# Optimization experiments

Measured on AMD Instinct MI355X. Metric: run time of the kernel, lower is better.

## Reference

```python
import jax, jax.numpy as jnp
import numpy as np

TEMP_UPDATE = 1e-05
EPS = 1e-12  # torch F.normalize eps


def _l2norm(x, axis):
    n = jnp.sqrt(jnp.sum(x * x, axis=axis, keepdims=True))
    return x / jnp.maximum(n, EPS)


def setup_inputs() -> dict:
    key = jax.random.key(0)
    k1, k2 = jax.random.split(key)
    query = jax.random.normal(k1, (64, 256, 512), dtype=jnp.float32)
    keys = jax.random.normal(k2, (2048, 512), dtype=jnp.float32)
    return {"query": query, "keys": keys}


def reference(query, keys):
    bs, t, d = query.shape
    m = keys.shape[0]
    # F.normalize(query, dim=2)
    q = _l2norm(query, axis=2)
    qr = q.reshape(bs * t, d)                      # [N, d]
    score = qr @ keys.T                            # [N, m]
    score_query = jax.nn.softmax(score, axis=0)    # softmax over queries per slot
    score_memory = jax.nn.softmax(score, axis=1)   # softmax over slots per query
    # topk(1) over memory dim -> argmax slot per query
    g = jnp.argmax(score_memory, axis=1)           # [N] int
    col_max = jnp.max(score_query, axis=0)         # [m]
    # weight per query: score_query[n, g_n] / max(score_query[:, g_n])
    w = jnp.take_along_axis(score_query, g[:, None], axis=1)[:, 0] / col_max[g]
    # fused scatter-add replacing the per-slot python loop
    query_update = jax.ops.segment_sum(w[:, None] * qr, g, num_segments=m)  # [m, d]
    updated = _l2norm(TEMP_UPDATE * query_update + keys, axis=1)
    return jax.lax.stop_gradient(updated)  # original returns .detach()
```

## Files before the change

kernel.cpp:

```cpp
#include <hip/hip_runtime.h>
#include <math.h>

#define N_Q     16384
#define DDIM    512
#define M_SLOTS 2048
#define EPSN    1e-12f
#define TEMPU   1e-5f
#define KSCALE  25.4f
#define QSCALE  127.0f
#define INV_S   (1.0f / (127.0f * 25.4f))

typedef unsigned int u32;
typedef unsigned long long u64;
typedef __attribute__((ext_vector_type(4))) int i32x4;

__device__ __forceinline__ void gld_lds16(const void* g, void* l) {
    __builtin_amdgcn_global_load_lds(
        (const __attribute__((address_space(1))) u32*)(g),
        (__attribute__((address_space(3))) u32*)(l), 16, 0, 0);
}
__device__ __forceinline__ float block_reduce_sum_128(float v, float* sred, int t) {
    #pragma unroll
    for (int o = 32; o > 0; o >>= 1) v += __shfl_down(v, o, 64);
    if ((t & 63) == 0) sred[t >> 6] = v;
    __syncthreads();
    return sred[0] + sred[1];
}
__device__ __forceinline__ char q8(float x, float s) {
    int v = __float2int_rn(x * s);
    v = v < -127 ? -127 : (v > 127 ? 127 : v);
    return (char)v;
}

__global__ __launch_bounds__(128) void k_prep(const float* __restrict__ q,
                                              const float* __restrict__ keys,
                                              char* __restrict__ qi8,
                                              char* __restrict__ ki8) {
    __shared__ float sred[2];
    int b = blockIdx.x;
    int t = threadIdx.x;
    if (b < N_Q) {
        float4 v = ((const float4*)(q + (size_t)b * DDIM))[t];
        float ss = v.x * v.x + v.y * v.y + v.z * v.z + v.w * v.w;
        ss = block_reduce_sum_128(ss, sred, t);
        float s = QSCALE / fmaxf(sqrtf(ss), EPSN);
        char4 o;
        o.x = q8(v.x, s);
        o.y = q8(v.y, s);
        o.z = q8(v.z, s);
        o.w = q8(v.w, s);
        ((char4*)(qi8 + (size_t)b * DDIM))[t] = o;
    } else {
        int r = b - N_Q;
        float4 v = ((const float4*)(keys + (size_t)r * DDIM))[t];
        char4 o;
        o.x = q8(v.x, KSCALE);
        o.y = q8(v.y, KSCALE);
        o.z = q8(v.z, KSCALE);
        o.w = q8(v.w, KSCALE);
        ((char4*)(ki8 + (size_t)r * DDIM))[t] = o;
    }
}

__global__ __launch_bounds__(256) void k_score(const char* __restrict__ qi8,
                                               const char* __restrict__ ki8,
                                               u64* __restrict__ rowpack,
                                               int* __restrict__ colmax) {
    __shared__ char sA[2][128 * 64];
    __shared__ char sB[2][128 * 64];

    int t = threadIdx.x;
    int lane = t & 63;
    int wid = t >> 6;
    int wrow = wid >> 1;
    int wcol = wid & 1;
    int lr = lane & 15;
    int kc = lane >> 4;

    int n0 = blockIdx.y * 128;
    int j0 = blockIdx.x * 128;

    int srow = t >> 2;
    int scolB = (t & 3) * 16;

    const char* gA0 = qi8 + (size_t)(n0 + srow) * DDIM + scolB;
    const char* gA1 = qi8 + (size_t)(n0 + 64 + srow) * DDIM + scolB;
    const char* gB0 = ki8 + (size_t)(j0 + srow) * DDIM + scolB;
    const char* gB1 = ki8 + (size_t)(j0 + 64 + srow) * DDIM + scolB;

    i32x4 acc[4][4] = {};

#define STAGE(buf, k0)  do {                                   \
        gld_lds16(gA0 + (k0), &sA[buf][t * 16]);               \
        gld_lds16(gA1 + (k0), &sA[buf][4096 + t * 16]);        \
        gld_lds16(gB0 + (k0), &sB[buf][t * 16]);               \
        gld_lds16(gB1 + (k0), &sB[buf][4096 + t * 16]);        \
    } while (0)

    STAGE(0, 0);
    __syncthreads();

    #pragma unroll
    for (int kt = 0; kt < 8; ++kt) {
        const int cur = kt & 1;
        if (kt < 7) STAGE(cur ^ 1, (kt + 1) * 64);

        i32x4 a[4], b[4];
        #pragma unroll
        for (int i = 0; i < 4; ++i)
            a[i] = *(const i32x4*)&sA[cur][(wrow * 64 + i * 16 + lr) * 64 + kc * 16];
        #pragma unroll
        for (int j = 0; j < 4; ++j)
            b[j] = *(const i32x4*)&sB[cur][(wcol * 64 + j * 16 + lr) * 64 + kc * 16];
        #pragma unroll
        for (int i = 0; i < 4; ++i)
            #pragma unroll
            for (int j = 0; j < 4; ++j)
                acc[i][j] = __builtin_amdgcn_mfma_i32_16x16x64_i8(a[i], b[j], acc[i][j], 0, 0, 0);

        if (kt < 7) __syncthreads();
    }
#undef STAGE

    #pragma unroll
    for (int i = 0; i < 4; ++i) {
        #pragma unroll
        for (int r = 0; r < 4; ++r) {
            int v = acc[i][0][r];
            int c = j0 + wcol * 64 + lr;
            #pragma unroll
            for (int j = 1; j < 4; ++j) {
                int vj = acc[i][j][r];
                int cj = j0 + wcol * 64 + j * 16 + lr;
                if (vj > v) { v = vj; c = cj; }
            }
            #pragma unroll
            for (int off = 1; off < 16; off <<= 1) {
                int ov = __shfl_xor(v, off, 64);
                int oc = __shfl_xor(c, off, 64);
                if (ov > v || (ov == v && oc < c)) { v = ov; c = oc; }
            }
            if (lr == 0) {
                int grow = n0 + wrow * 64 + i * 16 + kc * 4 + r;
                u64 pk = ((u64)(u32)(v ^ 0x80000000) << 32) | (u64)(~(u32)c);
                atomicMax(rowpack + grow, pk);
            }
        }
    }
    #pragma unroll
    for (int j = 0; j < 4; ++j) {
        int m = acc[0][j][0];
        #pragma unroll
        for (int i = 0; i < 4; ++i)
            #pragma unroll
            for (int r = 0; r < 4; ++r) m = max(m, acc[i][j][r]);
        m = max(m, __shfl_xor(m, 16, 64));
        m = max(m, __shfl_xor(m, 32, 64));
        if (kc == 0) atomicMax(colmax + j0 + wcol * 64 + j * 16 + lr, m);
    }
}

__global__ __launch_bounds__(256) void k_hist(const u64* __restrict__ rowpack,
                                              u32* __restrict__ cnt) {
    int n = blockIdx.x * 256 + threadIdx.x;
    u64 p = rowpack[n];
    int g = (int)(~(u32)(p & 0xFFFFFFFFull));
    atomicAdd(cnt + g, 1u);
}

__global__ __launch_bounds__(256) void k_scan(const u32* __restrict__ cnt,
                                              u32* __restrict__ start,
                                              u32* __restrict__ cursor) {
    __shared__ u32 wsum[4];
    int t = threadIdx.x;
    int lane = t & 63, w = t >> 6;
    u32 local[8], s = 0;
    #pragma unroll
    for (int i = 0; i < 8; ++i) { local[i] = cnt[t * 8 + i]; s += local[i]; }
    u32 x = s;
    #pragma unroll
    for (int off = 1; off < 64; off <<= 1) {
        u32 y = __shfl_up(x, off, 64);
        if (lane >= off) x += y;
    }
    if (lane == 63) wsum[w] = x;
    __syncthreads();
    u32 base = 0;
    #pragma unroll
    for (int i = 0; i < 4; ++i) if (i < w) base += wsum[i];
    u32 run = base + x - s;
    #pragma unroll
    for (int i = 0; i < 8; ++i) {
        start[t * 8 + i] = run;
        cursor[t * 8 + i] = run;
        run += local[i];
    }
}

__global__ __launch_bounds__(256) void k_fill(const u64* __restrict__ rowpack,
                                              const int* __restrict__ colmax,
                                              u32* __restrict__ cursor,
                                              u32* __restrict__ perm,
                                              float* __restrict__ wval) {
    int n = blockIdx.x * 256 + threadIdx.x;
    u64 p = rowpack[n];
    int vi = (int)(((u32)(p >> 32)) ^ 0x80000000u);
    int g = (int)(~(u32)(p & 0xFFFFFFFFull));
    int cm = colmax[g];
    float w = expf((float)(vi - cm) * INV_S);
    u32 pos = atomicAdd(cursor + g, 1u);
    perm[pos] = (u32)n;
    wval[pos] = w;
}

__global__ __launch_bounds__(128) void k_gather_final(const char* __restrict__ qi8,
                                                      const u32* __restrict__ start,
                                                      const u32* __restrict__ cnt,
                                                      const u32* __restrict__ perm,
                                                      const float* __restrict__ wval,
                                                      const float* __restrict__ keys,
                                                      float* __restrict__ out) {
    __shared__ float sred[2];
    int j = blockIdx.x;
    int t = threadIdx.x;
    u32 s = start[j];
    u32 e = s + cnt[j];
    float ax = 0.f, ay = 0.f, az = 0.f, aw = 0.f;
    for (u32 i = s; i < e; ++i) {
        u32 n = perm[i];
        float wq = wval[i] * (1.0f / 127.0f);
        char4 q4 = ((const char4*)(qi8 + (size_t)n * DDIM))[t];
        ax = fmaf(wq, (float)q4.x, ax);
        ay = fmaf(wq, (float)q4.y, ay);
        az = fmaf(wq, (float)q4.z, az);
        aw = fmaf(wq, (float)q4.w, aw);
    }
    float4 k4 = ((const float4*)(keys + (size_t)j * DDIM))[t];
    float4 v;
    v.x = fmaf(TEMPU, ax, k4.x);
    v.y = fmaf(TEMPU, ay, k4.y);
    v.z = fmaf(TEMPU, az, k4.z);
    v.w = fmaf(TEMPU, aw, k4.w);
    float ss = v.x * v.x + v.y * v.y + v.z * v.z + v.w * v.w;
    ss = block_reduce_sum_128(ss, sred, t);
    float inv = 1.0f / fmaxf(sqrtf(ss), EPSN);
    v.x *= inv; v.y *= inv; v.z *= inv; v.w *= inv;
    ((float4*)(out + (size_t)j * DDIM))[t] = v;
}

extern "C" void kernel_launch(void* const* d_in, const int* in_sizes, int n_in,
                              void* d_out, int out_size, void* d_ws, size_t ws_size,
                              hipStream_t stream) {
    const float* query = (const float*)d_in[0];
    const float* keys  = (const float*)d_in[1];
    float* out = (float*)d_out;

    char* ws = (char*)d_ws;
    const size_t OFF_QI8   = 0;
    const size_t OFF_ROW   = 8388608;
    const size_t OFF_CNT   = OFF_ROW + 131072;
    const size_t OFF_CMAX  = OFF_CNT + 8192;
    const size_t OFF_START = OFF_CMAX + 8192;
    const size_t OFF_CUR   = OFF_START + 8192;
    const size_t OFF_PERM  = OFF_CUR + 8192;
    const size_t OFF_W     = OFF_PERM + 65536;
    const size_t OFF_KI8   = OFF_W + 65536;

    char*   qi8    = ws + OFF_QI8;
    u64*    rowpack= (u64*)(ws + OFF_ROW);
    u32*    cnt    = (u32*)(ws + OFF_CNT);
    int*    cmax   = (int*)(ws + OFF_CMAX);
    u32*    start  = (u32*)(ws + OFF_START);
    u32*    cursor = (u32*)(ws + OFF_CUR);
    u32*    perm   = (u32*)(ws + OFF_PERM);
    float*  wval   = (float*)(ws + OFF_W);
    char*   ki8    = ws + OFF_KI8;

    hipMemsetAsync(ws + OFF_ROW, 0, 131072 + 8192, stream);
    hipMemsetAsync(ws + OFF_CMAX, 0x80, 8192, stream);

    k_prep<<<N_Q + M_SLOTS, 128, 0, stream>>>(query, keys, qi8, ki8);

    dim3 g2(M_SLOTS / 128, N_Q / 128);
    k_score<<<g2, 256, 0, stream>>>(qi8, ki8, rowpack, cmax);

    k_hist<<<N_Q / 256, 256, 0, stream>>>(rowpack, cnt);
    k_scan<<<1, 256, 0, stream>>>(cnt, start, cursor);
    k_fill<<<N_Q / 256, 256, 0, stream>>>(rowpack, cmax, cursor, perm, wval);
    k_gather_final<<<M_SLOTS, 128, 0, stream>>>(qi8, start, cnt, perm, wval, keys, out);
}
```

Before: 86.97 us.

## Triple-buffer score GEMM loads and fuse hist/scan/fill into one LDS sort kernel

```diff
diff --git a/kernel.cpp b/kernel.cpp
--- a/kernel.cpp
+++ b/kernel.cpp
@@ -65,9 +65,9 @@
 __global__ __launch_bounds__(256) void k_score(const char* __restrict__ qi8,
                                                const char* __restrict__ ki8,
                                                u64* __restrict__ rowpack,
-                                               int* __restrict__ colmax) {
-    __shared__ char sA[2][128 * 64];
-    __shared__ char sB[2][128 * 64];
+                                               u32* __restrict__ colmax) {
+    __shared__ char sA[3][128 * 64];
+    __shared__ char sB[3][128 * 64];
 
     int t = threadIdx.x;
     int lane = t & 63;
@@ -98,12 +98,15 @@
     } while (0)
 
     STAGE(0, 0);
-    __syncthreads();
+    STAGE(1, 64);
+    asm volatile("s_waitcnt vmcnt(4)" ::: "memory");
+    __builtin_amdgcn_s_barrier();
+    __builtin_amdgcn_sched_barrier(0);
 
     #pragma unroll
     for (int kt = 0; kt < 8; ++kt) {
-        const int cur = kt & 1;
-        if (kt < 7) STAGE(cur ^ 1, (kt + 1) * 64);
+        const int cur = kt % 3;
+        if (kt < 6) STAGE((kt + 2) % 3, (kt + 2) * 64);
 
         i32x4 a[4], b[4];
         #pragma unroll
@@ -118,7 +121,12 @@
             for (int j = 0; j < 4; ++j)
                 acc[i][j] = __builtin_amdgcn_mfma_i32_16x16x64_i8(a[i], b[j], acc[i][j], 0, 0, 0);
 
-        if (kt < 7) __syncthreads();
+        if (kt < 6)       asm volatile("s_waitcnt vmcnt(4)" ::: "memory");
+        else if (kt == 6) asm volatile("s_waitcnt vmcnt(0)" ::: "memory");
+        if (kt < 7) {
+            __builtin_amdgcn_s_barrier();
+            __builtin_amdgcn_sched_barrier(0);
+        }
     }
 #undef STAGE
 
@@ -156,27 +164,38 @@
             for (int r = 0; r < 4; ++r) m = max(m, acc[i][j][r]);
         m = max(m, __shfl_xor(m, 16, 64));
         m = max(m, __shfl_xor(m, 32, 64));
-        if (kc == 0) atomicMax(colmax + j0 + wcol * 64 + j * 16 + lr, m);
-    }
-}
-
-__global__ __launch_bounds__(256) void k_hist(const u64* __restrict__ rowpack,
-                                              u32* __restrict__ cnt) {
-    int n = blockIdx.x * 256 + threadIdx.x;
-    u64 p = rowpack[n];
-    int g = (int)(~(u32)(p & 0xFFFFFFFFull));
-    atomicAdd(cnt + g, 1u);
-}
-
-__global__ __launch_bounds__(256) void k_scan(const u32* __restrict__ cnt,
-                                              u32* __restrict__ start,
-                                              u32* __restrict__ cursor) {
-    __shared__ u32 wsum[4];
+        if (kc == 0) atomicMax(colmax + j0 + wcol * 64 + j * 16 + lr,
+                               (u32)m ^ 0x80000000u);
+    }
+}
+
+__global__ __launch_bounds__(1024) void k_sort(const u64* __restrict__ rowpack,
+                                               const u32* __restrict__ colmax,
+                                               u32* __restrict__ start_g,
+                                               u32* __restrict__ cnt_g,
+                                               u32* __restrict__ perm,
+                                               float* __restrict__ wval) {
+    __shared__ u32 scnt[M_SLOTS];
+    __shared__ u32 scur[M_SLOTS];
+    __shared__ u32 wsum[16];
     int t = threadIdx.x;
     int lane = t & 63, w = t >> 6;
-    u32 local[8], s = 0;
-    #pragma unroll
-    for (int i = 0; i < 8; ++i) { local[i] = cnt[t * 8 + i]; s += local[i]; }
+
+    scnt[t] = 0;
+    scnt[t + 1024] = 0;
+    __syncthreads();
+
+    #pragma unroll
+    for (int i = 0; i < 16; ++i) {
+        int n = i * 1024 + t;
+        u64 p = rowpack[n];
+        int g = (int)(~(u32)(p & 0xFFFFFFFFull));
+        atomicAdd(&scnt[g], 1u);
+    }
+    __syncthreads();
+
+    u32 c0 = scnt[2 * t], c1 = scnt[2 * t + 1];
+    u32 s = c0 + c1;
     u32 x = s;
     #pragma unroll
     for (int off = 1; off < 64; off <<= 1) {
@@ -185,32 +204,33 @@
     }
     if (lane == 63) wsum[w] = x;
     __syncthreads();
-    u32 base = 0;
-    #pragma unroll
-    for (int i = 0; i < 4; ++i) if (i < w) base += wsum[i];
-    u32 run = base + x - s;
-    #pragma unroll
-    for (int i = 0; i < 8; ++i) {
-        start[t * 8 + i] = run;
-        cursor[t * 8 + i] = run;
-        run += local[i];
-    }
-}
-
-__global__ __launch_bounds__(256) void k_fill(const u64* __restrict__ rowpack,
-                                              const int* __restrict__ colmax,
-                                              u32* __restrict__ cursor,
-                                              u32* __restrict__ perm,
-                                              float* __restrict__ wval) {
-    int n = blockIdx.x * 256 + threadIdx.x;
-    u64 p = rowpack[n];
-    int vi = (int)(((u32)(p >> 32)) ^ 0x80000000u);
-    int g = (int)(~(u32)(p & 0xFFFFFFFFull));
-    int cm = colmax[g];
-    float w = expf((float)(vi - cm) * INV_S);
-    u32 pos = atomicAdd(cursor + g, 1u);
-    perm[pos] = (u32)n;
-    wval[pos] = w;
+    if (t == 0) {
+        u32 a = 0;
+        #pragma unroll
+        for (int i = 0; i < 16; ++i) { u32 v = wsum[i]; wsum[i] = a; a += v; }
+    }
+    __syncthreads();
+    u32 ex = wsum[w] + x - s;
+    scur[2 * t]     = ex;
+    scur[2 * t + 1] = ex + c0;
+    start_g[2 * t]     = ex;
+    start_g[2 * t + 1] = ex + c0;
+    cnt_g[2 * t]     = c0;
+    cnt_g[2 * t + 1] = c1;
+    __syncthreads();
+
+    #pragma unroll
+    for (int i = 0; i < 16; ++i) {
+        int n = i * 1024 + t;
+        u64 p = rowpack[n];
+        int vi = (int)(((u32)(p >> 32)) ^ 0x80000000u);
+        int g = (int)(~(u32)(p & 0xFFFFFFFFull));
+        int cm = (int)(colmax[g] ^ 0x80000000u);
+        float wq = expf((float)(vi - cm) * INV_S);
+        u32 pos = atomicAdd(&scur[g], 1u);
+        perm[pos] = (u32)n;
+        wval[pos] = wq;
+    }
 }
 
 __global__ __launch_bounds__(128) void k_gather_final(const char* __restrict__ qi8,
@@ -258,34 +278,29 @@
     char* ws = (char*)d_ws;
     const size_t OFF_QI8   = 0;
     const size_t OFF_ROW   = 8388608;
-    const size_t OFF_CNT   = OFF_ROW + 131072;
-    const size_t OFF_CMAX  = OFF_CNT + 8192;
+    const size_t OFF_CMAX  = OFF_ROW + 131072;
     const size_t OFF_START = OFF_CMAX + 8192;
-    const size_t OFF_CUR   = OFF_START + 8192;
-    const size_t OFF_PERM  = OFF_CUR + 8192;
+    const size_t OFF_CNT   = OFF_START + 8192;
+    const size_t OFF_PERM  = OFF_CNT + 8192;
     const size_t OFF_W     = OFF_PERM + 65536;
     const size_t OFF_KI8   = OFF_W + 65536;
 
     char*   qi8    = ws + OFF_QI8;
     u64*    rowpack= (u64*)(ws + OFF_ROW);
+    u32*    cmax   = (u32*)(ws + OFF_CMAX);
+    u32*    start  = (u32*)(ws + OFF_START);
     u32*    cnt    = (u32*)(ws + OFF_CNT);
-    int*    cmax   = (int*)(ws + OFF_CMAX);
-    u32*    start  = (u32*)(ws + OFF_START);
-    u32*    cursor = (u32*)(ws + OFF_CUR);
     u32*    perm   = (u32*)(ws + OFF_PERM);
     float*  wval   = (float*)(ws + OFF_W);
     char*   ki8    = ws + OFF_KI8;
 
     hipMemsetAsync(ws + OFF_ROW, 0, 131072 + 8192, stream);
-    hipMemsetAsync(ws + OFF_CMAX, 0x80, 8192, stream);
 
     k_prep<<<N_Q + M_SLOTS, 128, 0, stream>>>(query, keys, qi8, ki8);
 
     dim3 g2(M_SLOTS / 128, N_Q / 128);
     k_score<<<g2, 256, 0, stream>>>(qi8, ki8, rowpack, cmax);
 
-    k_hist<<<N_Q / 256, 256, 0, stream>>>(rowpack, cnt);
-    k_scan<<<1, 256, 0, stream>>>(cnt, start, cursor);
-    k_fill<<<N_Q / 256, 256, 0, stream>>>(rowpack, cmax, cursor, perm, wval);
+    k_sort<<<1, 1024, 0, stream>>>(rowpack, cmax, start, cnt, perm, wval);
     k_gather_final<<<M_SLOTS, 128, 0, stream>>>(qi8, start, cnt, perm, wval, keys, out);
 }
```

Measured after the change: 103.0 us. 18.4% more time.

## Stage full key tile in LDS once and stream query fragments from registers

Applied to the files above, without the earlier changes.

```diff
diff --git a/kernel.cpp b/kernel.cpp
--- a/kernel.cpp
+++ b/kernel.cpp
@@ -65,9 +65,8 @@
 __global__ __launch_bounds__(256) void k_score(const char* __restrict__ qi8,
                                                const char* __restrict__ ki8,
                                                u64* __restrict__ rowpack,
-                                               int* __restrict__ colmax) {
-    __shared__ char sA[2][128 * 64];
-    __shared__ char sB[2][128 * 64];
+                                               u32* __restrict__ colmax) {
+    __shared__ char sB[128 * 512];
 
     int t = threadIdx.x;
     int lane = t & 63;
@@ -80,47 +79,46 @@
     int n0 = blockIdx.y * 128;
     int j0 = blockIdx.x * 128;
 
-    int srow = t >> 2;
-    int scolB = (t & 3) * 16;
-
-    const char* gA0 = qi8 + (size_t)(n0 + srow) * DDIM + scolB;
-    const char* gA1 = qi8 + (size_t)(n0 + 64 + srow) * DDIM + scolB;
-    const char* gB0 = ki8 + (size_t)(j0 + srow) * DDIM + scolB;
-    const char* gB1 = ki8 + (size_t)(j0 + 64 + srow) * DDIM + scolB;
+    #pragma unroll
+    for (int i = 0; i < 16; ++i) {
+        int m = i * 256 + t;
+        int row = m >> 5;
+        int slot = m & 31;
+        int gcol = (slot * 16) ^ ((row & 15) << 4);
+        gld_lds16(ki8 + (size_t)(j0 + row) * DDIM + gcol, &sB[m * 16]);
+    }
+    asm volatile("s_waitcnt vmcnt(0)" ::: "memory");
+    __syncthreads();
+
+    const char* ga[4];
+    #pragma unroll
+    for (int i = 0; i < 4; ++i)
+        ga[i] = qi8 + (size_t)(n0 + wrow * 64 + i * 16 + lr) * DDIM + kc * 16;
 
     i32x4 acc[4][4] = {};
-
-#define STAGE(buf, k0)  do {                                   \
-        gld_lds16(gA0 + (k0), &sA[buf][t * 16]);               \
-        gld_lds16(gA1 + (k0), &sA[buf][4096 + t * 16]);        \
-        gld_lds16(gB0 + (k0), &sB[buf][t * 16]);               \
-        gld_lds16(gB1 + (k0), &sB[buf][4096 + t * 16]);        \
-    } while (0)
-
-    STAGE(0, 0);
-    __syncthreads();
+    i32x4 aP[4], aN[4];
+    #pragma unroll
+    for (int i = 0; i < 4; ++i) aP[i] = *(const i32x4*)(ga[i]);
 
     #pragma unroll
     for (int kt = 0; kt < 8; ++kt) {
-        const int cur = kt & 1;
-        if (kt < 7) STAGE(cur ^ 1, (kt + 1) * 64);
-
-        i32x4 a[4], b[4];
+        if (kt < 7) {
+            #pragma unroll
+            for (int i = 0; i < 4; ++i) aN[i] = *(const i32x4*)(ga[i] + (kt + 1) * 64);
+        }
+        i32x4 b[4];
+        #pragma unroll
+        for (int j = 0; j < 4; ++j)
+            b[j] = *(const i32x4*)&sB[(wcol * 64 + j * 16 + lr) * 512 +
+                                      ((kt * 64 + kc * 16) ^ (lr << 4))];
         #pragma unroll
         for (int i = 0; i < 4; ++i)
-            a[i] = *(const i32x4*)&sA[cur][(wrow * 64 + i * 16 + lr) * 64 + kc * 16];
-        #pragma unroll
-        for (int j = 0; j < 4; ++j)
-            b[j] = *(const i32x4*)&sB[cur][(wcol * 64 + j * 16 + lr) * 64 + kc * 16];
-        #pragma unroll
-        for (int i = 0; i < 4; ++i)
             #pragma unroll
             for (int j = 0; j < 4; ++j)
-                acc[i][j] = __builtin_amdgcn_mfma_i32_16x16x64_i8(a[i], b[j], acc[i][j], 0, 0, 0);
-
-        if (kt < 7) __syncthreads();
-    }
-#undef STAGE
+                acc[i][j] = __builtin_amdgcn_mfma_i32_16x16x64_i8(aP[i], b[j], acc[i][j], 0, 0, 0);
+        #pragma unroll
+        for (int i = 0; i < 4; ++i) aP[i] = aN[i];
+    }
 
     #pragma unroll
     for (int i = 0; i < 4; ++i) {
@@ -156,7 +154,8 @@
             for (int r = 0; r < 4; ++r) m = max(m, acc[i][j][r]);
         m = max(m, __shfl_xor(m, 16, 64));
         m = max(m, __shfl_xor(m, 32, 64));
-        if (kc == 0) atomicMax(colmax + j0 + wcol * 64 + j * 16 + lr, m);
+        if (kc == 0) atomicMax(colmax + j0 + wcol * 64 + j * 16 + lr,
+                               (u32)m ^ 0x80000000u);
     }
 }
 
@@ -198,7 +197,7 @@
 }
 
 __global__ __launch_bounds__(256) void k_fill(const u64* __restrict__ rowpack,
-                                              const int* __restrict__ colmax,
+                                              const u32* __restrict__ colmax,
                                               u32* __restrict__ cursor,
                                               u32* __restrict__ perm,
                                               float* __restrict__ wval) {
@@ -206,7 +205,7 @@
     u64 p = rowpack[n];
     int vi = (int)(((u32)(p >> 32)) ^ 0x80000000u);
     int g = (int)(~(u32)(p & 0xFFFFFFFFull));
-    int cm = colmax[g];
+    int cm = (int)(colmax[g] ^ 0x80000000u);
     float w = expf((float)(vi - cm) * INV_S);
     u32 pos = atomicAdd(cursor + g, 1u);
     perm[pos] = (u32)n;
@@ -258,9 +257,9 @@
     char* ws = (char*)d_ws;
     const size_t OFF_QI8   = 0;
     const size_t OFF_ROW   = 8388608;
-    const size_t OFF_CNT   = OFF_ROW + 131072;
-    const size_t OFF_CMAX  = OFF_CNT + 8192;
-    const size_t OFF_START = OFF_CMAX + 8192;
+    const size_t OFF_CMAX  = OFF_ROW + 131072;
+    const size_t OFF_CNT   = OFF_CMAX + 8192;
+    const size_t OFF_START = OFF_CNT + 8192;
     const size_t OFF_CUR   = OFF_START + 8192;
     const size_t OFF_PERM  = OFF_CUR + 8192;
     const size_t OFF_W     = OFF_PERM + 65536;
@@ -268,16 +267,15 @@
 
     char*   qi8    = ws + OFF_QI8;
     u64*    rowpack= (u64*)(ws + OFF_ROW);
+    u32*    cmax   = (u32*)(ws + OFF_CMAX);
     u32*    cnt    = (u32*)(ws + OFF_CNT);
-    int*    cmax   = (int*)(ws + OFF_CMAX);
     u32*    start  = (u32*)(ws + OFF_START);
     u32*    cursor = (u32*)(ws + OFF_CUR);
     u32*    perm   = (u32*)(ws + OFF_PERM);
     float*  wval   = (float*)(ws + OFF_W);
     char*   ki8    = ws + OFF_KI8;
 
-    hipMemsetAsync(ws + OFF_ROW, 0, 131072 + 8192, stream);
-    hipMemsetAsync(ws + OFF_CMAX, 0x80, 8192, stream);
+    hipMemsetAsync(ws + OFF_ROW, 0, 131072 + 8192 + 8192, stream);
 
     k_prep<<<N_Q + M_SLOTS, 128, 0, stream>>>(query, keys, qi8, ki8);
 
```

New measurement: 101.9 us. +17.2%, slower.

## Enlarge score GEMM tile to 256x256 with triple-buffered LDS pipeline

Applied to the files above, without the earlier changes.

```diff
diff --git a/kernel.cpp b/kernel.cpp
--- a/kernel.cpp
+++ b/kernel.cpp
@@ -62,68 +62,76 @@
     }
 }
 
-__global__ __launch_bounds__(256) void k_score(const char* __restrict__ qi8,
-                                               const char* __restrict__ ki8,
-                                               u64* __restrict__ rowpack,
-                                               int* __restrict__ colmax) {
-    __shared__ char sA[2][128 * 64];
-    __shared__ char sB[2][128 * 64];
+__global__ __launch_bounds__(512, 2) void k_score(const char* __restrict__ qi8,
+                                                  const char* __restrict__ ki8,
+                                                  u64* __restrict__ rowpack,
+                                                  u32* __restrict__ colmax) {
+    __shared__ char sA[3][256 * 64];
+    __shared__ char sB[3][256 * 64];
 
     int t = threadIdx.x;
     int lane = t & 63;
     int wid = t >> 6;
-    int wrow = wid >> 1;
-    int wcol = wid & 1;
+    int wrow = wid >> 2;
+    int wcol = wid & 3;
     int lr = lane & 15;
     int kc = lane >> 4;
 
-    int n0 = blockIdx.y * 128;
-    int j0 = blockIdx.x * 128;
+    int j0 = blockIdx.x * 256;
+    int n0 = blockIdx.y * 256;
 
     int srow = t >> 2;
     int scolB = (t & 3) * 16;
 
     const char* gA0 = qi8 + (size_t)(n0 + srow) * DDIM + scolB;
-    const char* gA1 = qi8 + (size_t)(n0 + 64 + srow) * DDIM + scolB;
+    const char* gA1 = qi8 + (size_t)(n0 + 128 + srow) * DDIM + scolB;
     const char* gB0 = ki8 + (size_t)(j0 + srow) * DDIM + scolB;
-    const char* gB1 = ki8 + (size_t)(j0 + 64 + srow) * DDIM + scolB;
-
-    i32x4 acc[4][4] = {};
+    const char* gB1 = ki8 + (size_t)(j0 + 128 + srow) * DDIM + scolB;
+
+    i32x4 acc[8][4] = {};
 
 #define STAGE(buf, k0)  do {                                   \
         gld_lds16(gA0 + (k0), &sA[buf][t * 16]);               \
-        gld_lds16(gA1 + (k0), &sA[buf][4096 + t * 16]);        \
+        gld_lds16(gA1 + (k0), &sA[buf][8192 + t * 16]);        \
         gld_lds16(gB0 + (k0), &sB[buf][t * 16]);               \
-        gld_lds16(gB1 + (k0), &sB[buf][4096 + t * 16]);        \
+        gld_lds16(gB1 + (k0), &sB[buf][8192 + t * 16]);        \
     } while (0)
 
     STAGE(0, 0);
-    __syncthreads();
+    STAGE(1, 64);
+    asm volatile("s_waitcnt vmcnt(4)" ::: "memory");
+    __builtin_amdgcn_s_barrier();
+    __builtin_amdgcn_sched_barrier(0);
 
     #pragma unroll
     for (int kt = 0; kt < 8; ++kt) {
-        const int cur = kt & 1;
-        if (kt < 7) STAGE(cur ^ 1, (kt + 1) * 64);
-
-        i32x4 a[4], b[4];
-        #pragma unroll
-        for (int i = 0; i < 4; ++i)
-            a[i] = *(const i32x4*)&sA[cur][(wrow * 64 + i * 16 + lr) * 64 + kc * 16];
+        const int cur = kt % 3;
+        if (kt < 6) STAGE((kt + 2) % 3, (kt + 2) * 64);
+
+        i32x4 a[8], b[4];
+        #pragma unroll
+        for (int i = 0; i < 8; ++i)
+            a[i] = *(const i32x4*)&sA[cur][(wrow * 128 + i * 16 + lr) * 64 + kc * 16];
         #pragma unroll
         for (int j = 0; j < 4; ++j)
             b[j] = *(const i32x4*)&sB[cur][(wcol * 64 + j * 16 + lr) * 64 + kc * 16];
         #pragma unroll
-        for (int i = 0; i < 4; ++i)
+        for (int i = 0; i < 8; ++i)
             #pragma unroll
             for (int j = 0; j < 4; ++j)
                 acc[i][j] = __builtin_amdgcn_mfma_i32_16x16x64_i8(a[i], b[j], acc[i][j], 0, 0, 0);
 
-        if (kt < 7) __syncthreads();
+        if (kt < 6)       asm volatile("s_waitcnt vmcnt(4)" ::: "memory");
+        else if (kt == 6) asm volatile("s_waitcnt vmcnt(0)" ::: "memory");
+        if (kt < 7) {
+            __builtin_amdgcn_s_barrier();
+            __builtin_amdgcn_sched_barrier(0);
+        }
     }
 #undef STAGE
 
     #pragma unroll
-    for (int i = 0; i < 4; ++i) {
+    for (int i = 0; i < 8; ++i) {
         #pragma unroll
         for (int r = 0; r < 4; ++r) {
             int v = acc[i][0][r];
@@ -141,7 +149,7 @@
                 if (ov > v || (ov == v && oc < c)) { v = ov; c = oc; }
             }
             if (lr == 0) {
-                int grow = n0 + wrow * 64 + i * 16 + kc * 4 + r;
+                int grow = n0 + wrow * 128 + i * 16 + kc * 4 + r;
                 u64 pk = ((u64)(u32)(v ^ 0x80000000) << 32) | (u64)(~(u32)c);
                 atomicMax(rowpack + grow, pk);
             }
@@ -151,12 +159,13 @@
     for (int j = 0; j < 4; ++j) {
         int m = acc[0][j][0];
         #pragma unroll
-        for (int i = 0; i < 4; ++i)
+        for (int i = 0; i < 8; ++i)
             #pragma unroll
             for (int r = 0; r < 4; ++r) m = max(m, acc[i][j][r]);
         m = max(m, __shfl_xor(m, 16, 64));
         m = max(m, __shfl_xor(m, 32, 64));
-        if (kc == 0) atomicMax(colmax + j0 + wcol * 64 + j * 16 + lr, m);
+        if (kc == 0) atomicMax(colmax + j0 + wcol * 64 + j * 16 + lr,
+                               (u32)m ^ 0x80000000u);
     }
 }
 
@@ -198,7 +207,7 @@
 }
 
 __global__ __launch_bounds__(256) void k_fill(const u64* __restrict__ rowpack,
-                                              const int* __restrict__ colmax,
+                                              const u32* __restrict__ colmax,
                                               u32* __restrict__ cursor,
                                               u32* __restrict__ perm,
                                               float* __restrict__ wval) {
@@ -206,7 +215,7 @@
     u64 p = rowpack[n];
     int vi = (int)(((u32)(p >> 32)) ^ 0x80000000u);
     int g = (int)(~(u32)(p & 0xFFFFFFFFull));
-    int cm = colmax[g];
+    int cm = (int)(colmax[g] ^ 0x80000000u);
     float w = expf((float)(vi - cm) * INV_S);
     u32 pos = atomicAdd(cursor + g, 1u);
     perm[pos] = (u32)n;
@@ -258,9 +267,9 @@
     char* ws = (char*)d_ws;
     const size_t OFF_QI8   = 0;
     const size_t OFF_ROW   = 8388608;
-    const size_t OFF_CNT   = OFF_ROW + 131072;
-    const size_t OFF_CMAX  = OFF_CNT + 8192;
-    const size_t OFF_START = OFF_CMAX + 8192;
+    const size_t OFF_CMAX  = OFF_ROW + 131072;
+    const size_t OFF_CNT   = OFF_CMAX + 8192;
+    const size_t OFF_START = OFF_CNT + 8192;
     const size_t OFF_CUR   = OFF_START + 8192;
     const size_t OFF_PERM  = OFF_CUR + 8192;
     const size_t OFF_W     = OFF_PERM + 65536;
@@ -268,21 +277,20 @@
 
     char*   qi8    = ws + OFF_QI8;
     u64*    rowpack= (u64*)(ws + OFF_ROW);
+    u32*    cmax   = (u32*)(ws + OFF_CMAX);
     u32*    cnt    = (u32*)(ws + OFF_CNT);
-    int*    cmax   = (int*)(ws + OFF_CMAX);
     u32*    start  = (u32*)(ws + OFF_START);
     u32*    cursor = (u32*)(ws + OFF_CUR);
     u32*    perm   = (u32*)(ws + OFF_PERM);
     float*  wval   = (float*)(ws + OFF_W);
     char*   ki8    = ws + OFF_KI8;
 
-    hipMemsetAsync(ws + OFF_ROW, 0, 131072 + 8192, stream);
-    hipMemsetAsync(ws + OFF_CMAX, 0x80, 8192, stream);
+    hipMemsetAsync(ws + OFF_ROW, 0, 131072 + 8192 + 8192, stream);
 
     k_prep<<<N_Q + M_SLOTS, 128, 0, stream>>>(query, keys, qi8, ki8);
 
-    dim3 g2(M_SLOTS / 128, N_Q / 128);
-    k_score<<<g2, 256, 0, stream>>>(qi8, ki8, rowpack, cmax);
+    dim3 g2(M_SLOTS / 256, N_Q / 256);
+    k_score<<<g2, 512, 0, stream>>>(qi8, ki8, rowpack, cmax);
 
     k_hist<<<N_Q / 256, 256, 0, stream>>>(rowpack, cnt);
     k_scan<<<1, 256, 0, stream>>>(cnt, start, cursor);
```

After: 83.72 us. 1.04x faster.
